# Kernel optimization log

Measured on AMD Instinct MI355X. Metric: run time of the kernel, lower is better.

Reference implementation:

```python
import jax, jax.numpy as jnp
import numpy as np
from jax import lax

K, S, P = 3, 2, 1          # kernel, stride, padding
MIN_P, MAX_P = 1 + 1e-20, 110 + 1e-10
SCALE = 1.0                 # side_branch_scale
EPS = 1e-12


def setup_inputs() -> dict:
    key = jax.random.key(0)
    k1, k2, k3, k4 = jax.random.split(key, 4)
    B, C, H, W = 8, 256, 128, 128
    bottom = jax.random.uniform(k1, (B, C, H, W), dtype=jnp.float32)
    w1 = jax.random.normal(k2, (C, 1, K, K), dtype=jnp.float32) * 0.1  # depthwise conv weight (OIHW, I=1)
    a1 = jnp.full((C,), 0.25, dtype=jnp.float32)                       # PReLU slope, init 0.25
    w2 = jax.random.normal(k3, (C,), dtype=jnp.float32) * 0.1          # depthwise 1x1 conv weight
    b2 = jnp.full((C,), 70.0, dtype=jnp.float32) + 0.5 * jax.random.normal(k4, (C,), dtype=jnp.float32)  # init_bias=70
    return {"bottom": bottom, "w1": w1, "a1": a1, "w2": w2, "b2": b2}


def _exponent_branch(bottom, w1, a1, w2, b2):
    # bottom_0_max over H,W of |x|, +1; normalize; detach
    m = jnp.max(jnp.abs(bottom), axis=(2, 3), keepdims=True) + 1.0
    x = lax.stop_gradient(bottom / m * SCALE)
    C = bottom.shape[1]
    # depthwise KxK conv, stride S, padding P, no bias
    x = lax.conv_general_dilated(
        x, w1, window_strides=(S, S), padding=((P, P), (P, P)),
        dimension_numbers=("NCHW", "OIHW", "NCHW"), feature_group_count=C)
    # PReLU (per-channel)
    x = jnp.where(x > 0, x, a1[None, :, None, None] * x)
    # depthwise 1x1 conv with bias == per-channel affine
    x = x * w2[None, :, None, None] + b2[None, :, None, None]
    # Hardtanh clamp -> exponent p in [min_p, max_p]
    return jnp.clip(x, MIN_P, MAX_P)


def _p_pooling(bottom, pexp):
    # Windowed generalized power-mean with spatially-varying exponent p:
    #   out = (mean_k relu(x_k)^p)^(1/p), windows KxK stride S pad P (zero pad)
    B, C, H, W = bottom.shape
    Ho = (H + 2 * P - K) // S + 1
    Wo = (W + 2 * P - K) // S + 1
    xp = jnp.maximum(bottom, 0.0)
    xpad = jnp.pad(xp, ((0, 0), (0, 0), (P, P), (P, P)))
    # gather the K*K shifted strided views: [K*K, B, C, Ho, Wo]
    patches = jnp.stack([
        xpad[:, :, i:i + S * Ho:S, j:j + S * Wo:S]
        for i in range(K) for j in range(K)
    ], axis=0)
    mean_pow = jnp.mean(patches ** pexp[None], axis=0)
    return (mean_pow + EPS) ** (1.0 / pexp)


def reference(bottom, w1, a1, w2, b2):
    pexp = _exponent_branch(bottom, w1, a1, w2, b2)
    res = _p_pooling(bottom, pexp)
    return res, pexp
```

## Files before the change

kernel.cpp:

```cpp
#include <hip/hip_runtime.h>
#include <hip/hip_bf16.h>


#define HW 16384
#define N_OUT 8388608

__device__ __forceinline__ float hw_log2(float x) { return __builtin_amdgcn_logf(x); }
__device__ __forceinline__ float hw_exp2(float x) { return __builtin_amdgcn_exp2f(x); }
__device__ __forceinline__ float hw_rcp(float x)  { return __builtin_amdgcn_rcpf(x); }

__global__ __launch_bounds__(1024, 8) void fused_ppool_kernel(
    const float* __restrict__ bottom,
    const float* __restrict__ w1,
    const float* __restrict__ a1,
    const float* __restrict__ w2,
    const float* __restrict__ b2,
    float* __restrict__ out) {
    __shared__ float plane[HW];
    __shared__ float smax[16];

    const int bc   = blockIdx.x;
    const int c    = bc & 255;
    const int t    = threadIdx.x;
    const int wid  = t >> 6;
    const int lane = t & 63;

    const float4* src = reinterpret_cast<const float4*>(bottom + (size_t)bc * HW);
    float4* pl4 = reinterpret_cast<float4*>(plane);
    float mx = 0.f;
    #pragma unroll
    for (int k = 0; k < 4; ++k) {
        float4 v = src[t + k * 1024];
        pl4[t + k * 1024] = v;
        mx = fmaxf(mx, fmaxf(fmaxf(fabsf(v.x), fabsf(v.y)),
                             fmaxf(fabsf(v.z), fabsf(v.w))));
    }
    #pragma unroll
    for (int off = 32; off; off >>= 1)
        mx = fmaxf(mx, __shfl_down(mx, off, 64));
    if (lane == 0) smax[wid] = mx;
    __syncthreads();

    float m = 0.f;
    #pragma unroll
    for (int k = 0; k < 16; ++k) m = fmaxf(m, smax[k]);
    const float inv_m = hw_rcp(m + 1.0f);

    float wk[9];
    #pragma unroll
    for (int k = 0; k < 9; ++k) wk[k] = w1[c * 9 + k];
    const float slope = a1[c];
    const float ww2   = w2[c];
    const float bb2   = b2[c];

    float* outres = out + (size_t)bc * 4096;
    float* outp   = out + N_OUT + (size_t)bc * 4096;

    #pragma unroll
    for (int rr = 0; rr < 4; ++rr) {
        const int ho = wid + rr * 16;
        float xw[3][3];
        #pragma unroll
        for (int r = 0; r < 3; ++r) {
            const int hi = 2 * ho - 1 + r;
            float x0 = 0.f, x1 = 0.f, xm = 0.f;
            if ((unsigned)hi < 128u) {
                float2 v = *reinterpret_cast<const float2*>(&plane[hi * 128 + lane * 2]);
                x0 = v.x; x1 = v.y;
                xm = __shfl_up(x1, 1, 64);
                if (lane == 0) xm = 0.f;
            }
            xw[r][0] = xm; xw[r][1] = x0; xw[r][2] = x1;
        }

        float v = 0.f;
        #pragma unroll
        for (int r = 0; r < 3; ++r)
            #pragma unroll
            for (int j = 0; j < 3; ++j)
                v += wk[r * 3 + j] * xw[r][j];
        v *= inv_m;
        v = v > 0.f ? v : slope * v;
        float p = v * ww2 + bb2;
        p = fminf(fmaxf(p, 1.0f), 110.0f);

        float s = 0.f;
        #pragma unroll
        for (int r = 0; r < 3; ++r) {
            #pragma unroll
            for (int j = 0; j < 3; ++j) {
                float x = fmaxf(xw[r][j], 0.f);
                float e = hw_exp2(p * hw_log2(x));
                s += (x > 0.f) ? e : 0.f;
            }
        }
        float mp  = s * (1.0f / 9.0f) + 1e-12f;
        float res = hw_exp2(hw_log2(mp) * hw_rcp(p));

        outres[ho * 64 + lane] = res;
        outp  [ho * 64 + lane] = p;
    }
}

extern "C" void kernel_launch(void* const* d_in, const int* in_sizes, int n_in,
                              void* d_out, int out_size, void* d_ws, size_t ws_size,
                              hipStream_t stream) {
    const float* bottom = (const float*)d_in[0];
    const float* w1     = (const float*)d_in[1];
    const float* a1     = (const float*)d_in[2];
    const float* w2     = (const float*)d_in[3];
    const float* b2     = (const float*)d_in[4];
    float* out = (float*)d_out;

    fused_ppool_kernel<<<2048, 1024, 0, stream>>>(bottom, w1, a1, w2, b2, out);
}
```

Before: 42.78 us.

## Process four planes per block with register prefetch of next plane

Each block now loops over four channel planes with 512 threads. While the current plane is written to shared memory and reduced, the next plane is loaded into registers. This overlaps global loads with compute and makes the grid a single persistent-like wave. In exchange it halves threads per block and holds more registers per thread, which may reduce latency hiding.

```diff
diff --git a/kernel.cpp b/kernel.cpp
--- a/kernel.cpp
+++ b/kernel.cpp
@@ -4,12 +4,13 @@
 
 #define HW 16384
 #define N_OUT 8388608
+#define PPB 4
 
 __device__ __forceinline__ float hw_log2(float x) { return __builtin_amdgcn_logf(x); }
 __device__ __forceinline__ float hw_exp2(float x) { return __builtin_amdgcn_exp2f(x); }
 __device__ __forceinline__ float hw_rcp(float x)  { return __builtin_amdgcn_rcpf(x); }
 
-__global__ __launch_bounds__(1024, 8) void fused_ppool_kernel(
+__global__ __launch_bounds__(512, 4) void fused_ppool_pipe(
     const float* __restrict__ bottom,
     const float* __restrict__ w1,
     const float* __restrict__ a1,
@@ -17,88 +18,105 @@
     const float* __restrict__ b2,
     float* __restrict__ out) {
     __shared__ float plane[HW];
-    __shared__ float smax[16];
+    __shared__ float smax[8];
 
-    const int bc   = blockIdx.x;
-    const int c    = bc & 255;
     const int t    = threadIdx.x;
     const int wid  = t >> 6;
     const int lane = t & 63;
+    const int bc0  = blockIdx.x * PPB;
 
-    const float4* src = reinterpret_cast<const float4*>(bottom + (size_t)bc * HW);
+    float4 r[8];
+    {
+        const float4* s0 = reinterpret_cast<const float4*>(bottom + (size_t)bc0 * HW);
+        #pragma unroll
+        for (int k = 0; k < 8; ++k) r[k] = s0[t + k * 512];
+    }
     float4* pl4 = reinterpret_cast<float4*>(plane);
-    float mx = 0.f;
-    #pragma unroll
-    for (int k = 0; k < 4; ++k) {
-        float4 v = src[t + k * 1024];
-        pl4[t + k * 1024] = v;
-        mx = fmaxf(mx, fmaxf(fmaxf(fabsf(v.x), fabsf(v.y)),
-                             fmaxf(fabsf(v.z), fabsf(v.w))));
-    }
-    #pragma unroll
-    for (int off = 32; off; off >>= 1)
-        mx = fmaxf(mx, __shfl_down(mx, off, 64));
-    if (lane == 0) smax[wid] = mx;
-    __syncthreads();
 
-    float m = 0.f;
-    #pragma unroll
-    for (int k = 0; k < 16; ++k) m = fmaxf(m, smax[k]);
-    const float inv_m = hw_rcp(m + 1.0f);
+    for (int pi = 0; pi < PPB; ++pi) {
+        const int bc = bc0 + pi;
+        const int c  = bc & 255;
 
-    float wk[9];
-    #pragma unroll
-    for (int k = 0; k < 9; ++k) wk[k] = w1[c * 9 + k];
-    const float slope = a1[c];
-    const float ww2   = w2[c];
-    const float bb2   = b2[c];
+        __syncthreads();
 
-    float* outres = out + (size_t)bc * 4096;
-    float* outp   = out + N_OUT + (size_t)bc * 4096;
-
-    #pragma unroll
-    for (int rr = 0; rr < 4; ++rr) {
-        const int ho = wid + rr * 16;
-        float xw[3][3];
+        float mx = 0.f;
         #pragma unroll
-        for (int r = 0; r < 3; ++r) {
-            const int hi = 2 * ho - 1 + r;
-            float x0 = 0.f, x1 = 0.f, xm = 0.f;
-            if ((unsigned)hi < 128u) {
-                float2 v = *reinterpret_cast<const float2*>(&plane[hi * 128 + lane * 2]);
-                x0 = v.x; x1 = v.y;
-                xm = __shfl_up(x1, 1, 64);
-                if (lane == 0) xm = 0.f;
-            }
-            xw[r][0] = xm; xw[r][1] = x0; xw[r][2] = x1;
+        for (int k = 0; k < 8; ++k) {
+            float4 v = r[k];
+            pl4[t + k * 512] = v;
+            mx = fmaxf(mx, fmaxf(fmaxf(fabsf(v.x), fabsf(v.y)),
+                                 fmaxf(fabsf(v.z), fabsf(v.w))));
         }
 
-        float v = 0.f;
+        if (pi + 1 < PPB) {
+            const float4* sn = reinterpret_cast<const float4*>(bottom + (size_t)(bc + 1) * HW);
+            #pragma unroll
+            for (int k = 0; k < 8; ++k) r[k] = sn[t + k * 512];
+        }
+
         #pragma unroll
-        for (int r = 0; r < 3; ++r)
+        for (int off = 32; off; off >>= 1)
+            mx = fmaxf(mx, __shfl_down(mx, off, 64));
+        if (lane == 0) smax[wid] = mx;
+        __syncthreads();
+        float m = fmaxf(fmaxf(fmaxf(smax[0], smax[1]), fmaxf(smax[2], smax[3])),
+                        fmaxf(fmaxf(smax[4], smax[5]), fmaxf(smax[6], smax[7])));
+        const float inv_m = hw_rcp(m + 1.0f);
+
+        float wk[9];
+        #pragma unroll
+        for (int k = 0; k < 9; ++k) wk[k] = w1[c * 9 + k];
+        const float slope = a1[c];
+        const float ww2   = w2[c];
+        const float bb2   = b2[c];
+
+        float* outres = out + (size_t)bc * 4096;
+        float* outp   = out + N_OUT + (size_t)bc * 4096;
+
+        #pragma unroll
+        for (int rr = 0; rr < 8; ++rr) {
+            const int ho = wid * 8 + rr;
+            float xw[3][3];
             #pragma unroll
-            for (int j = 0; j < 3; ++j)
-                v += wk[r * 3 + j] * xw[r][j];
-        v *= inv_m;
-        v = v > 0.f ? v : slope * v;
-        float p = v * ww2 + bb2;
-        p = fminf(fmaxf(p, 1.0f), 110.0f);
+            for (int kr = 0; kr < 3; ++kr) {
+                const int hi = 2 * ho - 1 + kr;
+                float x0 = 0.f, x1 = 0.f, xm = 0.f;
+                if ((unsigned)hi < 128u) {
+                    float2 v2 = *reinterpret_cast<const float2*>(&plane[hi * 128 + lane * 2]);
+                    x0 = v2.x; x1 = v2.y;
+                    xm = __shfl_up(x1, 1, 64);
+                    if (lane == 0) xm = 0.f;
+                }
+                xw[kr][0] = xm; xw[kr][1] = x0; xw[kr][2] = x1;
+            }
 
-        float s = 0.f;
-        #pragma unroll
-        for (int r = 0; r < 3; ++r) {
+            float v = 0.f;
             #pragma unroll
-            for (int j = 0; j < 3; ++j) {
-                float x = fmaxf(xw[r][j], 0.f);
-                float e = hw_exp2(p * hw_log2(x));
-                s += (x > 0.f) ? e : 0.f;
+            for (int kr = 0; kr < 3; ++kr)
+                #pragma unroll
+                for (int j = 0; j < 3; ++j)
+                    v += wk[kr * 3 + j] * xw[kr][j];
+            v *= inv_m;
+            v = v > 0.f ? v : slope * v;
+            float p = v * ww2 + bb2;
+            p = fminf(fmaxf(p, 1.0f), 110.0f);
+
+            float s = 0.f;
+            #pragma unroll
+            for (int kr = 0; kr < 3; ++kr) {
+                #pragma unroll
+                for (int j = 0; j < 3; ++j) {
+                    float x = fmaxf(xw[kr][j], 0.f);
+                    float e = hw_exp2(p * hw_log2(x));
+                    s += (x > 0.f) ? e : 0.f;
+                }
             }
+            float mp  = s * (1.0f / 9.0f) + 1e-12f;
+            float res = hw_exp2(hw_log2(mp) * hw_rcp(p));
+
+            outres[ho * 64 + lane] = res;
+            outp  [ho * 64 + lane] = p;
         }
-        float mp  = s * (1.0f / 9.0f) + 1e-12f;
-        float res = hw_exp2(hw_log2(mp) * hw_rcp(p));
-
-        outres[ho * 64 + lane] = res;
-        outp  [ho * 64 + lane] = p;
     }
 }
 
@@ -112,5 +130,5 @@
     const float* b2     = (const float*)d_in[4];
     float* out = (float*)d_out;
 
-    fused_ppool_kernel<<<2048, 1024, 0, stream>>>(bottom, w1, a1, w2, b2, out);
+    fused_ppool_pipe<<<2048 / PPB, 512, 0, stream>>>(bottom, w1, a1, w2, b2, out);
 }
```

Result: slower. 56.74 us (+32.6%).

## Drop LDS plane staging, reread input from L2 with 256-thread blocks and row reuse

Applied to the files above, without the earlier changes.

The kernel no longer copies each 128x128 plane into 64KB of shared memory. The max-abs pass reads global memory directly, and the pooling pass rereads the plane through L2 cache. Blocks shrink to 256 threads, each wave handling 16 consecutive output rows and carrying the shared boundary input row forward in registers. This frees LDS and should raise occupancy, at the cost of a second pass over global/L2 memory. The x>0 select is dropped, relying on exp2(p*log2(0)) evaluating to zero.

```diff
diff --git a/kernel.cpp b/kernel.cpp
--- a/kernel.cpp
+++ b/kernel.cpp
@@ -9,41 +9,50 @@
 __device__ __forceinline__ float hw_exp2(float x) { return __builtin_amdgcn_exp2f(x); }
 __device__ __forceinline__ float hw_rcp(float x)  { return __builtin_amdgcn_rcpf(x); }
 
-__global__ __launch_bounds__(1024, 8) void fused_ppool_kernel(
+struct Row { float xm, x0, x1; };
+
+__device__ __forceinline__ Row load_row(const float* plane, int hi, int lane) {
+    float2 v = *reinterpret_cast<const float2*>(plane + hi * 128 + lane * 2);
+    float xm = __shfl_up(v.y, 1, 64);
+    if (lane == 0) xm = 0.f;
+    Row r; r.xm = xm; r.x0 = v.x; r.x1 = v.y; return r;
+}
+
+__global__ __launch_bounds__(256, 8) void fused_ppool_l2(
     const float* __restrict__ bottom,
     const float* __restrict__ w1,
     const float* __restrict__ a1,
     const float* __restrict__ w2,
     const float* __restrict__ b2,
     float* __restrict__ out) {
-    __shared__ float plane[HW];
-    __shared__ float smax[16];
+    __shared__ float smax[4];
 
-    const int bc   = blockIdx.x;
-    const int c    = bc & 255;
     const int t    = threadIdx.x;
     const int wid  = t >> 6;
     const int lane = t & 63;
+    const int bc   = blockIdx.x;
+    const int c    = bc & 255;
 
-    const float4* src = reinterpret_cast<const float4*>(bottom + (size_t)bc * HW);
-    float4* pl4 = reinterpret_cast<float4*>(plane);
-    float mx = 0.f;
+    const float* plane = bottom + (size_t)bc * HW;
+
+    const float4* p4 = reinterpret_cast<const float4*>(plane);
+    float m0 = 0.f, m1 = 0.f;
     #pragma unroll
-    for (int k = 0; k < 4; ++k) {
-        float4 v = src[t + k * 1024];
-        pl4[t + k * 1024] = v;
-        mx = fmaxf(mx, fmaxf(fmaxf(fabsf(v.x), fabsf(v.y)),
-                             fmaxf(fabsf(v.z), fabsf(v.w))));
+    for (int k = 0; k < 16; k += 2) {
+        float4 a = p4[t + k * 256];
+        float4 b = p4[t + (k + 1) * 256];
+        m0 = fmaxf(m0, fmaxf(fmaxf(fabsf(a.x), fabsf(a.y)),
+                             fmaxf(fabsf(a.z), fabsf(a.w))));
+        m1 = fmaxf(m1, fmaxf(fmaxf(fabsf(b.x), fabsf(b.y)),
+                             fmaxf(fabsf(b.z), fabsf(b.w))));
     }
+    float mx = fmaxf(m0, m1);
     #pragma unroll
     for (int off = 32; off; off >>= 1)
         mx = fmaxf(mx, __shfl_down(mx, off, 64));
     if (lane == 0) smax[wid] = mx;
     __syncthreads();
-
-    float m = 0.f;
-    #pragma unroll
-    for (int k = 0; k < 16; ++k) m = fmaxf(m, smax[k]);
+    const float m = fmaxf(fmaxf(smax[0], smax[1]), fmaxf(smax[2], smax[3]));
     const float inv_m = hw_rcp(m + 1.0f);
 
     float wk[9];
@@ -56,49 +65,46 @@
     float* outres = out + (size_t)bc * 4096;
     float* outp   = out + N_OUT + (size_t)bc * 4096;
 
+    const int ho0 = wid * 16;
+    Row top;
+    {
+        const int hi = 2 * ho0 - 1;
+        if (hi >= 0) top = load_row(plane, hi, lane);
+        else { top.xm = 0.f; top.x0 = 0.f; top.x1 = 0.f; }
+    }
+
     #pragma unroll
-    for (int rr = 0; rr < 4; ++rr) {
-        const int ho = wid + rr * 16;
-        float xw[3][3];
-        #pragma unroll
-        for (int r = 0; r < 3; ++r) {
-            const int hi = 2 * ho - 1 + r;
-            float x0 = 0.f, x1 = 0.f, xm = 0.f;
-            if ((unsigned)hi < 128u) {
-                float2 v = *reinterpret_cast<const float2*>(&plane[hi * 128 + lane * 2]);
-                x0 = v.x; x1 = v.y;
-                xm = __shfl_up(x1, 1, 64);
-                if (lane == 0) xm = 0.f;
-            }
-            xw[r][0] = xm; xw[r][1] = x0; xw[r][2] = x1;
-        }
+    for (int rr = 0; rr < 16; ++rr) {
+        const int ho = ho0 + rr;
+        Row mid = load_row(plane, 2 * ho,     lane);
+        Row bot = load_row(plane, 2 * ho + 1, lane);
 
-        float v = 0.f;
-        #pragma unroll
-        for (int r = 0; r < 3; ++r)
-            #pragma unroll
-            for (int j = 0; j < 3; ++j)
-                v += wk[r * 3 + j] * xw[r][j];
+        float v = wk[0] * top.xm + wk[1] * top.x0 + wk[2] * top.x1
+                + wk[3] * mid.xm + wk[4] * mid.x0 + wk[5] * mid.x1
+                + wk[6] * bot.xm + wk[7] * bot.x0 + wk[8] * bot.x1;
         v *= inv_m;
         v = v > 0.f ? v : slope * v;
         float p = v * ww2 + bb2;
         p = fminf(fmaxf(p, 1.0f), 110.0f);
 
         float s = 0.f;
-        #pragma unroll
-        for (int r = 0; r < 3; ++r) {
-            #pragma unroll
-            for (int j = 0; j < 3; ++j) {
-                float x = fmaxf(xw[r][j], 0.f);
-                float e = hw_exp2(p * hw_log2(x));
-                s += (x > 0.f) ? e : 0.f;
-            }
-        }
+        s += hw_exp2(p * hw_log2(fmaxf(top.xm, 0.f)));
+        s += hw_exp2(p * hw_log2(fmaxf(top.x0, 0.f)));
+        s += hw_exp2(p * hw_log2(fmaxf(top.x1, 0.f)));
+        s += hw_exp2(p * hw_log2(fmaxf(mid.xm, 0.f)));
+        s += hw_exp2(p * hw_log2(fmaxf(mid.x0, 0.f)));
+        s += hw_exp2(p * hw_log2(fmaxf(mid.x1, 0.f)));
+        s += hw_exp2(p * hw_log2(fmaxf(bot.xm, 0.f)));
+        s += hw_exp2(p * hw_log2(fmaxf(bot.x0, 0.f)));
+        s += hw_exp2(p * hw_log2(fmaxf(bot.x1, 0.f)));
+
         float mp  = s * (1.0f / 9.0f) + 1e-12f;
         float res = hw_exp2(hw_log2(mp) * hw_rcp(p));
 
         outres[ho * 64 + lane] = res;
         outp  [ho * 64 + lane] = p;
+
+        top = bot;
     }
 }
 
@@ -112,5 +118,5 @@
     const float* b2     = (const float*)d_in[4];
     float* out = (float*)d_out;
 
-    fused_ppool_kernel<<<2048, 1024, 0, stream>>>(bottom, w1, a1, w2, b2, out);
+    fused_ppool_l2<<<2048, 256, 0, stream>>>(bottom, w1, a1, w2, b2, out);
 }
```

New measurement: 81.14 us. 1.9x slower.

## Drop LDS staging; each wave reads its own rows directly and reuses logs

Applied to the files above, without the earlier changes.

The 64KB shared-memory plane is removed. Each wave now owns four consecutive output rows and loads the nine overlapping input rows straight from global memory into registers. While loading, it computes the abs-max partial and accumulates the conv numerator before scaling by the later-known 1/max, since the conv is linear. log2 values are computed once per input element and shared across the overlapping windows, with the left neighbour's log taken by shuffle. This cuts LDS traffic and redundant transcendentals and frees LDS for higher occupancy, at the cost of more registers and uncoalesced row-overlap reads.

```diff
diff --git a/kernel.cpp b/kernel.cpp
--- a/kernel.cpp
+++ b/kernel.cpp
@@ -4,47 +4,28 @@
 
 #define HW 16384
 #define N_OUT 8388608
+#define NEG_INF (-__builtin_inff())
 
 __device__ __forceinline__ float hw_log2(float x) { return __builtin_amdgcn_logf(x); }
 __device__ __forceinline__ float hw_exp2(float x) { return __builtin_amdgcn_exp2f(x); }
 __device__ __forceinline__ float hw_rcp(float x)  { return __builtin_amdgcn_rcpf(x); }
 
-__global__ __launch_bounds__(1024, 8) void fused_ppool_kernel(
+__global__ __launch_bounds__(1024, 8) void fused_ppool_v10(
     const float* __restrict__ bottom,
     const float* __restrict__ w1,
     const float* __restrict__ a1,
     const float* __restrict__ w2,
     const float* __restrict__ b2,
     float* __restrict__ out) {
-    __shared__ float plane[HW];
     __shared__ float smax[16];
 
-    const int bc   = blockIdx.x;
-    const int c    = bc & 255;
     const int t    = threadIdx.x;
     const int wid  = t >> 6;
     const int lane = t & 63;
+    const int bc   = blockIdx.x;
+    const int c    = bc & 255;
 
-    const float4* src = reinterpret_cast<const float4*>(bottom + (size_t)bc * HW);
-    float4* pl4 = reinterpret_cast<float4*>(plane);
-    float mx = 0.f;
-    #pragma unroll
-    for (int k = 0; k < 4; ++k) {
-        float4 v = src[t + k * 1024];
-        pl4[t + k * 1024] = v;
-        mx = fmaxf(mx, fmaxf(fmaxf(fabsf(v.x), fabsf(v.y)),
-                             fmaxf(fabsf(v.z), fabsf(v.w))));
-    }
-    #pragma unroll
-    for (int off = 32; off; off >>= 1)
-        mx = fmaxf(mx, __shfl_down(mx, off, 64));
-    if (lane == 0) smax[wid] = mx;
-    __syncthreads();
-
-    float m = 0.f;
-    #pragma unroll
-    for (int k = 0; k < 16; ++k) m = fmaxf(m, smax[k]);
-    const float inv_m = hw_rcp(m + 1.0f);
+    const float* plane = bottom + (size_t)bc * HW;
 
     float wk[9];
     #pragma unroll
@@ -53,50 +34,72 @@
     const float ww2   = w2[c];
     const float bb2   = b2[c];
 
+    const int ho0   = wid * 4;
+    const int hbase = 2 * ho0 - 1;
+
+    float lx0[9], lx1[9];
+    float A[4];
+    A[0] = A[1] = A[2] = A[3] = 0.f;
+    float mx = 0.f;
+
+    #pragma unroll
+    for (int r = 0; r < 9; ++r) {
+        const int hi = hbase + r;
+        float a = 0.f, b = 0.f;
+        if (hi >= 0) {
+            float2 v = *reinterpret_cast<const float2*>(plane + hi * 128 + lane * 2);
+            a = v.x; b = v.y;
+        }
+        mx = fmaxf(mx, fmaxf(fabsf(a), fabsf(b)));
+        float xm = __shfl_up(b, 1, 64);
+        if (lane == 0) xm = 0.f;
+        #pragma unroll
+        for (int rr = 0; rr < 4; ++rr) {
+            const int k = r - 2 * rr;
+            if (k >= 0 && k <= 2)
+                A[rr] += wk[3 * k] * xm + wk[3 * k + 1] * a + wk[3 * k + 2] * b;
+        }
+        lx0[r] = hw_log2(fmaxf(a, 0.f));
+        lx1[r] = hw_log2(fmaxf(b, 0.f));
+    }
+
+    #pragma unroll
+    for (int off = 32; off; off >>= 1)
+        mx = fmaxf(mx, __shfl_down(mx, off, 64));
+    if (lane == 0) smax[wid] = mx;
+    __syncthreads();
+    float mm = smax[0];
+    #pragma unroll
+    for (int k = 1; k < 16; ++k) mm = fmaxf(mm, smax[k]);
+    const float inv_m = hw_rcp(mm + 1.0f);
+
+    float lxm[9];
+    #pragma unroll
+    for (int r = 0; r < 9; ++r) {
+        float s = __shfl_up(lx1[r], 1, 64);
+        lxm[r] = (lane == 0) ? NEG_INF : s;
+    }
+
     float* outres = out + (size_t)bc * 4096;
     float* outp   = out + N_OUT + (size_t)bc * 4096;
 
     #pragma unroll
     for (int rr = 0; rr < 4; ++rr) {
-        const int ho = wid + rr * 16;
-        float xw[3][3];
-        #pragma unroll
-        for (int r = 0; r < 3; ++r) {
-            const int hi = 2 * ho - 1 + r;
-            float x0 = 0.f, x1 = 0.f, xm = 0.f;
-            if ((unsigned)hi < 128u) {
-                float2 v = *reinterpret_cast<const float2*>(&plane[hi * 128 + lane * 2]);
-                x0 = v.x; x1 = v.y;
-                xm = __shfl_up(x1, 1, 64);
-                if (lane == 0) xm = 0.f;
-            }
-            xw[r][0] = xm; xw[r][1] = x0; xw[r][2] = x1;
-        }
-
-        float v = 0.f;
-        #pragma unroll
-        for (int r = 0; r < 3; ++r)
-            #pragma unroll
-            for (int j = 0; j < 3; ++j)
-                v += wk[r * 3 + j] * xw[r][j];
-        v *= inv_m;
+        float v = A[rr] * inv_m;
         v = v > 0.f ? v : slope * v;
         float p = v * ww2 + bb2;
         p = fminf(fmaxf(p, 1.0f), 110.0f);
 
         float s = 0.f;
         #pragma unroll
-        for (int r = 0; r < 3; ++r) {
-            #pragma unroll
-            for (int j = 0; j < 3; ++j) {
-                float x = fmaxf(xw[r][j], 0.f);
-                float e = hw_exp2(p * hw_log2(x));
-                s += (x > 0.f) ? e : 0.f;
-            }
+        for (int k = 0; k < 3; ++k) {
+            const int r = 2 * rr + k;
+            s += hw_exp2(p * lxm[r]) + hw_exp2(p * lx0[r]) + hw_exp2(p * lx1[r]);
         }
         float mp  = s * (1.0f / 9.0f) + 1e-12f;
         float res = hw_exp2(hw_log2(mp) * hw_rcp(p));
 
+        const int ho = ho0 + rr;
         outres[ho * 64 + lane] = res;
         outp  [ho * 64 + lane] = p;
     }
@@ -112,5 +115,5 @@
     const float* b2     = (const float*)d_in[4];
     float* out = (float*)d_out;
 
-    fused_ppool_kernel<<<2048, 1024, 0, stream>>>(bottom, w1, a1, w2, b2, out);
+    fused_ppool_v10<<<2048, 1024, 0, stream>>>(bottom, w1, a1, w2, b2, out);
 }
```

Result: faster. 36.45 us (-14.8%).
